# Kernel tuning notes

Measured on AMD Instinct MI355X. Metric: run time of the kernel, lower is better.

## Reference

```python
import jax, jax.numpy as jnp
import numpy as np

INPUT_DIM = 512
N_TREES = 64
TREE_DEPTH = 3
N_LEAVES = 2 ** TREE_DEPTH      # 8
N_INTERNAL = 2 ** TREE_DEPTH - 1  # 7
PPT = N_INTERNAL * (INPUT_DIM + 1) + N_LEAVES * 2  # params per tree = 3607
BATCH = 65536


def setup_inputs() -> dict:
    key = jax.random.key(0)
    k1, k2, k3 = jax.random.split(key, 3)
    x = jax.random.normal(k1, (BATCH, INPUT_DIM), dtype=jnp.float32)
    tree_params = jax.random.normal(k2, (1, N_TREES * PPT), dtype=jnp.float32)
    tree_weights = jax.random.normal(k3, (1, N_TREES), dtype=jnp.float32)
    return {"x": x, "tree_params": tree_params, "tree_weights": tree_weights}


def reference(x, tree_params, tree_weights):
    # Unpack all trees at once: [T, ppt]
    p = tree_params[0].reshape(N_TREES, PPT)
    split_w = p[:, : N_INTERNAL * INPUT_DIM].reshape(N_TREES, N_INTERNAL, INPUT_DIM)
    split_b = p[:, N_INTERNAL * INPUT_DIM : N_INTERNAL * (INPUT_DIM + 1)]  # [T, I]
    leaf_logits = p[:, N_INTERNAL * (INPUT_DIM + 1) :].reshape(N_TREES, N_LEAVES, 2)

    # decisions: [B, T, I]
    decisions = jax.nn.sigmoid(jnp.einsum('bd,tid->bti', x, split_w) + split_b[None])

    # Replicate the original indexing quirk: leaf_probs column j (a tree NODE index)
    # gets factor d_i if j == 2i+1 (and j < n_leaves), (1-d_i) if j == 2i+2.
    # Column 0 remains 1.0; each other column gets exactly one factor.
    cols = []
    for j in range(N_LEAVES):
        if j == 0:
            cols.append(jnp.ones_like(decisions[:, :, 0]))
        elif j % 2 == 1:
            i = (j - 1) // 2
            cols.append(decisions[:, :, i] if i < N_INTERNAL else jnp.ones_like(decisions[:, :, 0]))
        else:
            i = (j - 2) // 2
            cols.append(1.0 - decisions[:, :, i] if i < N_INTERNAL else jnp.ones_like(decisions[:, :, 0]))
    leaf_probs = jnp.stack(cols, axis=-1)  # [B, T, L]
    leaf_probs = leaf_probs / (leaf_probs.sum(axis=-1, keepdims=True) + 1e-8)

    leaf_dist = jax.nn.softmax(leaf_logits, axis=-1)  # [T, L, 2]
    tree_out = jnp.einsum('btl,tlc->btc', leaf_probs, leaf_dist)  # [B, T, 2]
    return jnp.einsum('btc,t->bc', tree_out, tree_weights[0])  # [B, 2]
```

## Files before the change

### kernel.cpp

```cpp
#include <hip/hip_runtime.h>
#include <stdint.h>


#define KDIM 512
#define PPT 3607

typedef _Float16 f16x8 __attribute__((ext_vector_type(8)));
typedef float f32x4 __attribute__((ext_vector_type(4)));


__global__ __launch_bounds__(128) void prep_kernel(const float* __restrict__ p,
                                                   const float* __restrict__ tw,
                                                   _Float16* __restrict__ Wh,
                                                   float* __restrict__ biasN,
                                                   float* __restrict__ AB) {
    const int c = blockIdx.x;
    const int t = c >> 2, i = c & 3;
    const float* wsrc = p + t * PPT + i * KDIM;
    for (int k = threadIdx.x; k < KDIM; k += 128)
        Wh[c * KDIM + k] = (_Float16)wsrc[k];
    if (threadIdx.x == 0)
        biasN[c] = p[t * PPT + 7 * KDIM + i];
    if (threadIdx.x == 64 && c < 64) {
        const int tt = c;
        const float* lg = p + tt * PPT + 7 * 513;
        const float w = tw[tt];
        float ld[8][2];
#pragma unroll
        for (int j = 0; j < 8; ++j) {
            float a = lg[2 * j], b = lg[2 * j + 1];
            float m = fmaxf(a, b);
            float e0 = expf(a - m), e1 = expf(b - m);
            float s = e0 + e1;
            ld[j][0] = e0 / s; ld[j][1] = e1 / s;
        }
        float* o = AB + tt * 10;
#pragma unroll
        for (int cc = 0; cc < 2; ++cc) {
            o[0 + cc] = w * (ld[0][cc] + ld[2][cc] + ld[4][cc] + ld[6][cc]);
            o[2 + cc] = w * (ld[1][cc] - ld[2][cc]);
            o[4 + cc] = w * (ld[3][cc] - ld[4][cc]);
            o[6 + cc] = w * (ld[5][cc] - ld[6][cc]);
            o[8 + cc] = w * (ld[7][cc]);
        }
    }
}

#define BUF_STRIDE 32768
#define W_OFF 16384
#define EPI_STRIDE 260
#define AB_OFF 66560
#define PART_OFF 69120
#define LDS_BYTES 73216

__device__ __forceinline__ void gll16(const void* g, void* l) {
    __builtin_amdgcn_global_load_lds((const __attribute__((address_space(1))) uint32_t*)g,
                                     (__attribute__((address_space(3))) uint32_t*)l, 16, 0, 0);
}

__global__ __launch_bounds__(512, 4) void main_kernel(const float* __restrict__ X,
                                                      const _Float16* __restrict__ Wh,
                                                      const float* __restrict__ biasN,
                                                      const float* __restrict__ ABg,
                                                      float* __restrict__ out) {
    extern __shared__ char smem[];
    const int tid = threadIdx.x;
    const int lane = tid & 63;
    const int w = tid >> 6;
    const int wm = w >> 2;
    const int wn = w & 3;
    const int gr0 = blockIdx.x * 128;

    {
        float* abl = (float*)(smem + AB_OFF);
        for (int i = tid; i < 640; i += 512) abl[i] = ABg[i];
    }
    asm volatile("s_waitcnt vmcnt(0)" ::: "memory");

    const float* srcX[2];
    const _Float16* srcW[2];
    int ldoX[2], ldoW[2];
#pragma unroll
    for (int i = 0; i < 2; ++i) {
        int rowX = i * 64 + w * 8 + (lane >> 3);
        int cX = ((lane & 7) << 2) ^ ((rowX & 7) << 2);
        srcX[i] = X + (size_t)(gr0 + rowX) * KDIM + cX;
        ldoX[i] = (i * 512 + w * 64 + lane) * 16;
        int colW = i * 128 + w * 16 + (lane >> 2);
        int kW = ((lane & 3) << 3) ^ (((colW >> 1) & 3) << 3);
        srcW[i] = Wh + (size_t)colW * KDIM + kW;
        ldoW[i] = W_OFF + (i * 512 + w * 64 + lane) * 16;
    }

#define STAGE(kt, b) do {                                   \
        char* _bb = smem + (b) * BUF_STRIDE;                \
        gll16(srcX[0] + (kt) * 32, _bb + ldoX[0]);          \
        gll16(srcX[1] + (kt) * 32, _bb + ldoX[1]);          \
        gll16(srcW[0] + (kt) * 32, _bb + ldoW[0]);          \
        gll16(srcW[1] + (kt) * 32, _bb + ldoW[1]);          \
    } while (0)

    f32x4 acc[4][4];
#pragma unroll
    for (int rt = 0; rt < 4; ++rt)
#pragma unroll
        for (int nt = 0; nt < 4; ++nt)
            acc[rt][nt] = (f32x4){0.f, 0.f, 0.f, 0.f};

    const int kb = (lane >> 4) << 3;
    const int swA = (lane & 7) << 2;
    const int swB = ((lane >> 1) & 3) << 3;
    const int aRowBase = (wm * 64 + (lane & 15)) * 32;
    const int bColBase = (wn * 64 + (lane & 15)) * 32;

    STAGE(0, 0);

    for (int kt = 0; kt < 16; ++kt) {
        const int b = kt & 1;
        __builtin_amdgcn_s_barrier();
        if (kt < 15) {
            STAGE(kt + 1, b ^ 1);
            asm volatile("s_waitcnt vmcnt(4)" ::: "memory");
        } else {
            asm volatile("s_waitcnt vmcnt(0)" ::: "memory");
        }
        __builtin_amdgcn_s_barrier();
        asm volatile("" ::: "memory");

        const float* Xl = (const float*)(smem + b * BUF_STRIDE);
        const _Float16* Wl = (const _Float16*)(smem + b * BUF_STRIDE + W_OFF);

        f16x8 bfr[4];
#pragma unroll
        for (int nt = 0; nt < 4; ++nt)
            bfr[nt] = *(const f16x8*)&Wl[bColBase + nt * 512 + (kb ^ swB)];
#pragma unroll
        for (int rt = 0; rt < 4; ++rt) {
            float4 a0 = *(const float4*)&Xl[aRowBase + rt * 512 + (kb ^ swA)];
            float4 a1 = *(const float4*)&Xl[aRowBase + rt * 512 + ((kb + 4) ^ swA)];
            f16x8 af;
            af[0] = (_Float16)a0.x; af[1] = (_Float16)a0.y;
            af[2] = (_Float16)a0.z; af[3] = (_Float16)a0.w;
            af[4] = (_Float16)a1.x; af[5] = (_Float16)a1.y;
            af[6] = (_Float16)a1.z; af[7] = (_Float16)a1.w;
#pragma unroll
            for (int nt = 0; nt < 4; ++nt)
                acc[rt][nt] = __builtin_amdgcn_mfma_f32_16x16x32_f16(af, bfr[nt], acc[rt][nt], 0, 0, 0);
        }
    }

    __syncthreads();

    for (int p = 0; p < 2; ++p) {
        if (wm == p) {
            float bl[4];
#pragma unroll
            for (int nt = 0; nt < 4; ++nt) bl[nt] = biasN[wn * 64 + nt * 16 + (lane & 15)];
            float* ep = (float*)smem;
#pragma unroll
            for (int rt = 0; rt < 4; ++rt)
#pragma unroll
                for (int nt = 0; nt < 4; ++nt) {
                    const int col = wn * 64 + nt * 16 + (lane & 15);
#pragma unroll
                    for (int reg = 0; reg < 4; ++reg) {
                        const int rowl = rt * 16 + ((lane >> 4) << 2) + reg;
                        float z = acc[rt][nt][reg] + bl[nt];
                        ep[rowl * EPI_STRIDE + col] = __builtin_amdgcn_rcpf(1.f + __expf(-z));
                    }
                }
        }
        __syncthreads();
        {
            const float* ep = (const float*)smem;
            const float* abl = (const float*)(smem + AB_OFF);
            float* pb = (float*)(smem + PART_OFF);
            const int r = lane;
            float s0 = 0.f, s1 = 0.f;
#pragma unroll
            for (int j = 0; j < 8; ++j) {
                const int t = w * 8 + j;
                float4 dv = *(const float4*)&ep[r * EPI_STRIDE + t * 4];
                const float* abt = &abl[t * 10];
                float inv = __builtin_amdgcn_rcpf(4.f + dv.w + 1e-8f);
                s0 += (abt[0] + dv.x * abt[2] + dv.y * abt[4] + dv.z * abt[6] + dv.w * abt[8]) * inv;
                s1 += (abt[1] + dv.x * abt[3] + dv.y * abt[5] + dv.z * abt[7] + dv.w * abt[9]) * inv;
            }
            pb[(w * 64 + r) * 2 + 0] = s0;
            pb[(w * 64 + r) * 2 + 1] = s1;
        }
        __syncthreads();
        if (tid < 128) {
            const float* pb = (const float*)(smem + PART_OFF);
            const int r = tid >> 1, c = tid & 1;
            float s = 0.f;
#pragma unroll
            for (int g = 0; g < 8; ++g) s += pb[(g * 64 + r) * 2 + c];
            out[(size_t)(gr0 + p * 64 + r) * 2 + c] = s;
        }
        if (p == 0) __syncthreads();
    }
#undef STAGE
}

extern "C" void kernel_launch(void* const* d_in, const int* in_sizes, int n_in,
                              void* d_out, int out_size, void* d_ws, size_t ws_size,
                              hipStream_t stream) {
    const float* x  = (const float*)d_in[0];
    const float* tp = (const float*)d_in[1];
    const float* tw = (const float*)d_in[2];
    float* out = (float*)d_out;

    _Float16* Wh = (_Float16*)d_ws;
    float* biasN = (float*)((char*)d_ws + 262144);
    float* AB    = (float*)((char*)d_ws + 263168);

    (void)hipFuncSetAttribute((const void*)reinterpret_cast<const void*>(&main_kernel),
                              hipFuncAttributeMaxDynamicSharedMemorySize, LDS_BYTES);

    prep_kernel<<<256, 128, 0, stream>>>(tp, tw, Wh, biasN, AB);
    main_kernel<<<512, 512, LDS_BYTES, stream>>>(x, Wh, biasN, AB, out);
}
```

Baseline: 41.93 us.

## Load X through registers, convert to fp16 once, and triple-buffer W

X tiles now go from global memory into registers two stages ahead, are converted to fp16 once per thread, and are written to a smaller double-buffered LDS area. Each wave used to convert the fp32 LDS data itself, so the same values were converted repeatedly. W moves to a three-stage LDS ring loaded two iterations ahead, which allows a single barrier per k-step instead of two. The change trades higher register pressure and more complex vmcnt accounting for fewer barriers, less LDS traffic and fewer conversion instructions.

Result: no change. 42.37 us (+1.0%).

```diff
diff --git a/kernel.cpp b/kernel.cpp
--- a/kernel.cpp
+++ b/kernel.cpp
@@ -46,8 +46,9 @@
     }
 }
 
-#define BUF_STRIDE 32768
-#define W_OFF 16384
+#define XBUF_STRIDE 8192
+#define W_BASE 16384
+#define WBUF_STRIDE 16384
 #define EPI_STRIDE 260
 #define AB_OFF 66560
 #define PART_OFF 69120
@@ -56,6 +57,13 @@
 __device__ __forceinline__ void gll16(const void* g, void* l) {
     __builtin_amdgcn_global_load_lds((const __attribute__((address_space(1))) uint32_t*)g,
                                      (__attribute__((address_space(3))) uint32_t*)l, 16, 0, 0);
+}
+
+__device__ __forceinline__ f16x8 cvt8(float4 a, float4 b) {
+    f16x8 h;
+    h[0] = (_Float16)a.x; h[1] = (_Float16)a.y; h[2] = (_Float16)a.z; h[3] = (_Float16)a.w;
+    h[4] = (_Float16)b.x; h[5] = (_Float16)b.y; h[6] = (_Float16)b.z; h[7] = (_Float16)b.w;
+    return h;
 }
 
 __global__ __launch_bounds__(512, 4) void main_kernel(const float* __restrict__ X,
@@ -77,28 +85,24 @@
     }
     asm volatile("s_waitcnt vmcnt(0)" ::: "memory");
 
-    const float* srcX[2];
+    const float* Xrow = X + (size_t)(gr0 + (tid >> 2)) * KDIM + (tid & 3) * 8;
+    const int wOffX = ((tid >> 2) << 6) + ((((tid & 3) ^ ((tid >> 3) & 3))) << 4);
+
     const _Float16* srcW[2];
-    int ldoX[2], ldoW[2];
+    int dW[2];
 #pragma unroll
     for (int i = 0; i < 2; ++i) {
-        int rowX = i * 64 + w * 8 + (lane >> 3);
-        int cX = ((lane & 7) << 2) ^ ((rowX & 7) << 2);
-        srcX[i] = X + (size_t)(gr0 + rowX) * KDIM + cX;
-        ldoX[i] = (i * 512 + w * 64 + lane) * 16;
         int colW = i * 128 + w * 16 + (lane >> 2);
         int kW = ((lane & 3) << 3) ^ (((colW >> 1) & 3) << 3);
         srcW[i] = Wh + (size_t)colW * KDIM + kW;
-        ldoW[i] = W_OFF + (i * 512 + w * 64 + lane) * 16;
-    }
-
-#define STAGE(kt, b) do {                                   \
-        char* _bb = smem + (b) * BUF_STRIDE;                \
-        gll16(srcX[0] + (kt) * 32, _bb + ldoX[0]);          \
-        gll16(srcX[1] + (kt) * 32, _bb + ldoX[1]);          \
-        gll16(srcW[0] + (kt) * 32, _bb + ldoW[0]);          \
-        gll16(srcW[1] + (kt) * 32, _bb + ldoW[1]);          \
-    } while (0)
+        dW[i] = (i * 512 + w * 64 + lane) * 16;
+    }
+
+    const int kb = (lane >> 4) << 3;
+    const int kws = kb ^ (((lane >> 1) & 3) << 3);
+    const int bColBase = (wn * 64 + (lane & 15)) * 32;
+    const int aOff = ((lane & 15) << 6)
+                   + (((lane >> 4) ^ (((lane & 15) >> 1) & 3)) << 4);
 
     f32x4 acc[4][4];
 #pragma unroll
@@ -107,45 +111,52 @@
         for (int nt = 0; nt < 4; ++nt)
             acc[rt][nt] = (f32x4){0.f, 0.f, 0.f, 0.f};
 
-    const int kb = (lane >> 4) << 3;
-    const int swA = (lane & 7) << 2;
-    const int swB = ((lane >> 1) & 3) << 3;
-    const int aRowBase = (wm * 64 + (lane & 15)) * 32;
-    const int bColBase = (wn * 64 + (lane & 15)) * 32;
-
-    STAGE(0, 0);
-
+    float4 xr[2][2];
+
+    {
+        float4 x0a = *(const float4*)(Xrow + 0);
+        float4 x0b = *(const float4*)(Xrow + 4);
+        gll16(srcW[0] + 0 * 32, smem + W_BASE + 0 * WBUF_STRIDE + dW[0]);
+        gll16(srcW[1] + 0 * 32, smem + W_BASE + 0 * WBUF_STRIDE + dW[1]);
+        xr[1][0] = *(const float4*)(Xrow + 1 * 32);
+        xr[1][1] = *(const float4*)(Xrow + 1 * 32 + 4);
+        gll16(srcW[0] + 1 * 32, smem + W_BASE + 1 * WBUF_STRIDE + dW[0]);
+        gll16(srcW[1] + 1 * 32, smem + W_BASE + 1 * WBUF_STRIDE + dW[1]);
+        *(f16x8*)(smem + 0 * XBUF_STRIDE + wOffX) = cvt8(x0a, x0b);
+    }
+
+#pragma unroll 16
     for (int kt = 0; kt < 16; ++kt) {
-        const int b = kt & 1;
+        if (kt <= 13) {
+            xr[kt & 1][0] = *(const float4*)(Xrow + (kt + 2) * 32);
+            xr[kt & 1][1] = *(const float4*)(Xrow + (kt + 2) * 32 + 4);
+        }
+        if (kt <= 13)      asm volatile("s_waitcnt vmcnt(4)" ::: "memory");
+        else if (kt == 14) asm volatile("s_waitcnt vmcnt(2)" ::: "memory");
+        else               asm volatile("s_waitcnt vmcnt(0)" ::: "memory");
         __builtin_amdgcn_s_barrier();
-        if (kt < 15) {
-            STAGE(kt + 1, b ^ 1);
-            asm volatile("s_waitcnt vmcnt(4)" ::: "memory");
-        } else {
-            asm volatile("s_waitcnt vmcnt(0)" ::: "memory");
-        }
-        __builtin_amdgcn_s_barrier();
-        asm volatile("" ::: "memory");
-
-        const float* Xl = (const float*)(smem + b * BUF_STRIDE);
-        const _Float16* Wl = (const _Float16*)(smem + b * BUF_STRIDE + W_OFF);
-
-        f16x8 bfr[4];
-#pragma unroll
-        for (int nt = 0; nt < 4; ++nt)
-            bfr[nt] = *(const f16x8*)&Wl[bColBase + nt * 512 + (kb ^ swB)];
-#pragma unroll
-        for (int rt = 0; rt < 4; ++rt) {
-            float4 a0 = *(const float4*)&Xl[aRowBase + rt * 512 + (kb ^ swA)];
-            float4 a1 = *(const float4*)&Xl[aRowBase + rt * 512 + ((kb + 4) ^ swA)];
-            f16x8 af;
-            af[0] = (_Float16)a0.x; af[1] = (_Float16)a0.y;
-            af[2] = (_Float16)a0.z; af[3] = (_Float16)a0.w;
-            af[4] = (_Float16)a1.x; af[5] = (_Float16)a1.y;
-            af[6] = (_Float16)a1.z; af[7] = (_Float16)a1.w;
+        if (kt <= 13) {
+            char* wb = smem + W_BASE + ((kt + 2) % 3) * WBUF_STRIDE;
+            gll16(srcW[0] + (kt + 2) * 32, wb + dW[0]);
+            gll16(srcW[1] + (kt + 2) * 32, wb + dW[1]);
+        }
+        if (kt <= 14)
+            *(f16x8*)(smem + ((kt + 1) & 1) * XBUF_STRIDE + wOffX) =
+                cvt8(xr[(kt + 1) & 1][0], xr[(kt + 1) & 1][1]);
+        {
+            const _Float16* Wl = (const _Float16*)(smem + W_BASE + (kt % 3) * WBUF_STRIDE);
+            const char* Xl = smem + (kt & 1) * XBUF_STRIDE + wm * 4096;
+            f16x8 bfr[4];
 #pragma unroll
             for (int nt = 0; nt < 4; ++nt)
-                acc[rt][nt] = __builtin_amdgcn_mfma_f32_16x16x32_f16(af, bfr[nt], acc[rt][nt], 0, 0, 0);
+                bfr[nt] = *(const f16x8*)&Wl[bColBase + nt * 512 + kws];
+#pragma unroll
+            for (int rt = 0; rt < 4; ++rt) {
+                f16x8 af = *(const f16x8*)(Xl + rt * 1024 + aOff);
+#pragma unroll
+                for (int nt = 0; nt < 4; ++nt)
+                    acc[rt][nt] = __builtin_amdgcn_mfma_f32_16x16x32_f16(af, bfr[nt], acc[rt][nt], 0, 0, 0);
+            }
         }
     }
 
@@ -200,7 +211,6 @@
         }
         if (p == 0) __syncthreads();
     }
-#undef STAGE
 }
 
 extern "C" void kernel_launch(void* const* d_in, const int* in_sizes, int n_in,
```

## Keep split weights in registers and stream X through LDS as fp16

Applied to the files above, without the earlier changes.

Each wave now loads its 32 columns of fp16 split weights into registers once, for the whole K dimension. Blocks then stream 256 rows of X in 32-row panels: values are loaded to registers, converted to fp16 and written to a double-buffered swizzled LDS tile, and the MFMA and epilogue run per panel. This drops the per-k-step reload of W from LDS and halves X's LDS footprint. It also gives up the async global_load_lds pipeline, adds a large register cost (Wf is 128 VGPRs, with occupancy lowered to 2 blocks), and adds more barriers per panel.

Result: slower. 47.62 us (+13.6%).

```diff
diff --git a/kernel.cpp b/kernel.cpp
--- a/kernel.cpp
+++ b/kernel.cpp
@@ -4,10 +4,16 @@
 
 #define KDIM 512
 #define PPT 3607
+#define NP 8
+#define EPI_S 260
+#define E_OFF 65536
+#define P_OFF 98816
+#define P_S 34
+#define AB_OFF 103168
+#define LDS_BYTES 105728
 
 typedef _Float16 f16x8 __attribute__((ext_vector_type(8)));
 typedef float f32x4 __attribute__((ext_vector_type(4)));
-
 
 __global__ __launch_bounds__(128) void prep_kernel(const float* __restrict__ p,
                                                    const float* __restrict__ tw,
@@ -46,19 +52,14 @@
     }
 }
 
-#define BUF_STRIDE 32768
-#define W_OFF 16384
-#define EPI_STRIDE 260
-#define AB_OFF 66560
-#define PART_OFF 69120
-#define LDS_BYTES 73216
-
-__device__ __forceinline__ void gll16(const void* g, void* l) {
-    __builtin_amdgcn_global_load_lds((const __attribute__((address_space(1))) uint32_t*)g,
-                                     (__attribute__((address_space(3))) uint32_t*)l, 16, 0, 0);
-}
-
-__global__ __launch_bounds__(512, 4) void main_kernel(const float* __restrict__ X,
+__device__ __forceinline__ f16x8 cvt8(float4 a, float4 b) {
+    f16x8 h;
+    h[0] = (_Float16)a.x; h[1] = (_Float16)a.y; h[2] = (_Float16)a.z; h[3] = (_Float16)a.w;
+    h[4] = (_Float16)b.x; h[5] = (_Float16)b.y; h[6] = (_Float16)b.z; h[7] = (_Float16)b.w;
+    return h;
+}
+
+__global__ __launch_bounds__(512, 2) void main_kernel(const float* __restrict__ X,
                                                       const _Float16* __restrict__ Wh,
                                                       const float* __restrict__ biasN,
                                                       const float* __restrict__ ABg,
@@ -66,141 +67,124 @@
     extern __shared__ char smem[];
     const int tid = threadIdx.x;
     const int lane = tid & 63;
-    const int w = tid >> 6;
-    const int wm = w >> 2;
-    const int wn = w & 3;
-    const int gr0 = blockIdx.x * 128;
+    const int wn = tid >> 6;
+    const int r15 = lane & 15;
+    const int hi = lane >> 4;
+    const int gr0 = blockIdx.x * 256;
 
     {
         float* abl = (float*)(smem + AB_OFF);
         for (int i = tid; i < 640; i += 512) abl[i] = ABg[i];
     }
-    asm volatile("s_waitcnt vmcnt(0)" ::: "memory");
-
-    const float* srcX[2];
-    const _Float16* srcW[2];
-    int ldoX[2], ldoW[2];
-#pragma unroll
-    for (int i = 0; i < 2; ++i) {
-        int rowX = i * 64 + w * 8 + (lane >> 3);
-        int cX = ((lane & 7) << 2) ^ ((rowX & 7) << 2);
-        srcX[i] = X + (size_t)(gr0 + rowX) * KDIM + cX;
-        ldoX[i] = (i * 512 + w * 64 + lane) * 16;
-        int colW = i * 128 + w * 16 + (lane >> 2);
-        int kW = ((lane & 3) << 3) ^ (((colW >> 1) & 3) << 3);
-        srcW[i] = Wh + (size_t)colW * KDIM + kW;
-        ldoW[i] = W_OFF + (i * 512 + w * 64 + lane) * 16;
-    }
-
-#define STAGE(kt, b) do {                                   \
-        char* _bb = smem + (b) * BUF_STRIDE;                \
-        gll16(srcX[0] + (kt) * 32, _bb + ldoX[0]);          \
-        gll16(srcX[1] + (kt) * 32, _bb + ldoX[1]);          \
-        gll16(srcW[0] + (kt) * 32, _bb + ldoW[0]);          \
-        gll16(srcW[1] + (kt) * 32, _bb + ldoW[1]);          \
-    } while (0)
-
-    f32x4 acc[4][4];
-#pragma unroll
-    for (int rt = 0; rt < 4; ++rt)
-#pragma unroll
-        for (int nt = 0; nt < 4; ++nt)
-            acc[rt][nt] = (f32x4){0.f, 0.f, 0.f, 0.f};
-
-    const int kb = (lane >> 4) << 3;
-    const int swA = (lane & 7) << 2;
-    const int swB = ((lane >> 1) & 3) << 3;
-    const int aRowBase = (wm * 64 + (lane & 15)) * 32;
-    const int bColBase = (wn * 64 + (lane & 15)) * 32;
-
-    STAGE(0, 0);
-
-    for (int kt = 0; kt < 16; ++kt) {
-        const int b = kt & 1;
+
+    f16x8 Wf[16][2];
+#pragma unroll
+    for (int s = 0; s < 16; ++s)
+#pragma unroll
+        for (int ct = 0; ct < 2; ++ct)
+            Wf[s][ct] = *(const f16x8*)&Wh[(size_t)(wn * 32 + ct * 16 + r15) * KDIM + s * 32 + hi * 8];
+
+    float bl[2];
+#pragma unroll
+    for (int ct = 0; ct < 2; ++ct) bl[ct] = biasN[wn * 32 + ct * 16 + r15];
+
+    int srow[4], ldw[4];
+#pragma unroll
+    for (int i = 0; i < 4; ++i) {
+        int chunk = i * 512 + tid;
+        int row = chunk >> 6, g = chunk & 63;
+        srow[i] = chunk * 8;
+        ldw[i] = row * 1024 + ((g ^ (row & 15)) << 4);
+    }
+
+    const int aoff0 = r15 * 1024;
+    const int aoff1 = (16 + r15) * 1024;
+
+    const float* Xblk = X + (size_t)gr0 * KDIM;
+    float4 xr[8];
+
+#pragma unroll
+    for (int i = 0; i < 4; ++i) {
+        xr[2 * i]     = *(const float4*)(Xblk + srow[i]);
+        xr[2 * i + 1] = *(const float4*)(Xblk + srow[i] + 4);
+    }
+
+    for (int p = 0; p < NP; ++p) {
+        char* xb = smem + (p & 1) * 32768;
+#pragma unroll
+        for (int i = 0; i < 4; ++i)
+            *(f16x8*)(xb + ldw[i]) = cvt8(xr[2 * i], xr[2 * i + 1]);
+        if (p + 1 < NP) {
+            const float* Xp = Xblk + (size_t)(p + 1) * 32 * KDIM;
+#pragma unroll
+            for (int i = 0; i < 4; ++i) {
+                xr[2 * i]     = *(const float4*)(Xp + srow[i]);
+                xr[2 * i + 1] = *(const float4*)(Xp + srow[i] + 4);
+            }
+        }
+        asm volatile("s_waitcnt lgkmcnt(0)" ::: "memory");
         __builtin_amdgcn_s_barrier();
-        if (kt < 15) {
-            STAGE(kt + 1, b ^ 1);
-            asm volatile("s_waitcnt vmcnt(4)" ::: "memory");
-        } else {
-            asm volatile("s_waitcnt vmcnt(0)" ::: "memory");
-        }
+
+        f32x4 acc[2][2];
+#pragma unroll
+        for (int rt = 0; rt < 2; ++rt)
+#pragma unroll
+            for (int ct = 0; ct < 2; ++ct)
+                acc[rt][ct] = (f32x4){0.f, 0.f, 0.f, 0.f};
+#pragma unroll
+        for (int s = 0; s < 16; ++s) {
+            const int go = ((s * 4 + hi) ^ r15) << 4;
+            f16x8 a0 = *(const f16x8*)(xb + aoff0 + go);
+            f16x8 a1 = *(const f16x8*)(xb + aoff1 + go);
+            acc[0][0] = __builtin_amdgcn_mfma_f32_16x16x32_f16(a0, Wf[s][0], acc[0][0], 0, 0, 0);
+            acc[0][1] = __builtin_amdgcn_mfma_f32_16x16x32_f16(a0, Wf[s][1], acc[0][1], 0, 0, 0);
+            acc[1][0] = __builtin_amdgcn_mfma_f32_16x16x32_f16(a1, Wf[s][0], acc[1][0], 0, 0, 0);
+            acc[1][1] = __builtin_amdgcn_mfma_f32_16x16x32_f16(a1, Wf[s][1], acc[1][1], 0, 0, 0);
+        }
+
+        float* Ef = (float*)(smem + E_OFF);
+#pragma unroll
+        for (int rt = 0; rt < 2; ++rt)
+#pragma unroll
+            for (int ct = 0; ct < 2; ++ct) {
+                const int col = wn * 32 + ct * 16 + r15;
+#pragma unroll
+                for (int reg = 0; reg < 4; ++reg) {
+                    const int row = rt * 16 + hi * 4 + reg;
+                    float z = acc[rt][ct][reg] + bl[ct];
+                    Ef[row * EPI_S + col] = __builtin_amdgcn_rcpf(1.f + __expf(-z));
+                }
+            }
+        asm volatile("s_waitcnt lgkmcnt(0)" ::: "memory");
         __builtin_amdgcn_s_barrier();
-        asm volatile("" ::: "memory");
-
-        const float* Xl = (const float*)(smem + b * BUF_STRIDE);
-        const _Float16* Wl = (const _Float16*)(smem + b * BUF_STRIDE + W_OFF);
-
-        f16x8 bfr[4];
-#pragma unroll
-        for (int nt = 0; nt < 4; ++nt)
-            bfr[nt] = *(const f16x8*)&Wl[bColBase + nt * 512 + (kb ^ swB)];
-#pragma unroll
-        for (int rt = 0; rt < 4; ++rt) {
-            float4 a0 = *(const float4*)&Xl[aRowBase + rt * 512 + (kb ^ swA)];
-            float4 a1 = *(const float4*)&Xl[aRowBase + rt * 512 + ((kb + 4) ^ swA)];
-            f16x8 af;
-            af[0] = (_Float16)a0.x; af[1] = (_Float16)a0.y;
-            af[2] = (_Float16)a0.z; af[3] = (_Float16)a0.w;
-            af[4] = (_Float16)a1.x; af[5] = (_Float16)a1.y;
-            af[6] = (_Float16)a1.z; af[7] = (_Float16)a1.w;
-#pragma unroll
-            for (int nt = 0; nt < 4; ++nt)
-                acc[rt][nt] = __builtin_amdgcn_mfma_f32_16x16x32_f16(af, bfr[nt], acc[rt][nt], 0, 0, 0);
-        }
-    }
-
-    __syncthreads();
-
-    for (int p = 0; p < 2; ++p) {
-        if (wm == p) {
-            float bl[4];
-#pragma unroll
-            for (int nt = 0; nt < 4; ++nt) bl[nt] = biasN[wn * 64 + nt * 16 + (lane & 15)];
-            float* ep = (float*)smem;
-#pragma unroll
-            for (int rt = 0; rt < 4; ++rt)
-#pragma unroll
-                for (int nt = 0; nt < 4; ++nt) {
-                    const int col = wn * 64 + nt * 16 + (lane & 15);
-#pragma unroll
-                    for (int reg = 0; reg < 4; ++reg) {
-                        const int rowl = rt * 16 + ((lane >> 4) << 2) + reg;
-                        float z = acc[rt][nt][reg] + bl[nt];
-                        ep[rowl * EPI_STRIDE + col] = __builtin_amdgcn_rcpf(1.f + __expf(-z));
-                    }
-                }
-        }
-        __syncthreads();
         {
-            const float* ep = (const float*)smem;
             const float* abl = (const float*)(smem + AB_OFF);
-            float* pb = (float*)(smem + PART_OFF);
-            const int r = lane;
+            float* Pf = (float*)(smem + P_OFF);
+            const int row = tid >> 4, tg = tid & 15;
             float s0 = 0.f, s1 = 0.f;
 #pragma unroll
-            for (int j = 0; j < 8; ++j) {
-                const int t = w * 8 + j;
-                float4 dv = *(const float4*)&ep[r * EPI_STRIDE + t * 4];
+            for (int j = 0; j < 4; ++j) {
+                const int t = tg * 4 + j;
+                float4 dv = *(const float4*)&Ef[row * EPI_S + t * 4];
                 const float* abt = &abl[t * 10];
                 float inv = __builtin_amdgcn_rcpf(4.f + dv.w + 1e-8f);
                 s0 += (abt[0] + dv.x * abt[2] + dv.y * abt[4] + dv.z * abt[6] + dv.w * abt[8]) * inv;
                 s1 += (abt[1] + dv.x * abt[3] + dv.y * abt[5] + dv.z * abt[7] + dv.w * abt[9]) * inv;
             }
-            pb[(w * 64 + r) * 2 + 0] = s0;
-            pb[(w * 64 + r) * 2 + 1] = s1;
-        }
-        __syncthreads();
-        if (tid < 128) {
-            const float* pb = (const float*)(smem + PART_OFF);
-            const int r = tid >> 1, c = tid & 1;
+            Pf[row * P_S + tg * 2 + 0] = s0;
+            Pf[row * P_S + tg * 2 + 1] = s1;
+        }
+        asm volatile("s_waitcnt lgkmcnt(0)" ::: "memory");
+        __builtin_amdgcn_s_barrier();
+        if (tid < 64) {
+            const float* Pf = (const float*)(smem + P_OFF);
+            const int row = tid >> 1, c = tid & 1;
             float s = 0.f;
 #pragma unroll
-            for (int g = 0; g < 8; ++g) s += pb[(g * 64 + r) * 2 + c];
-            out[(size_t)(gr0 + p * 64 + r) * 2 + c] = s;
-        }
-        if (p == 0) __syncthreads();
-    }
-#undef STAGE
+            for (int tg = 0; tg < 16; ++tg) s += Pf[row * P_S + tg * 2 + c];
+            out[(size_t)(gr0 + p * 32 + row) * 2 + c] = s;
+        }
+    }
 }
 
 extern "C" void kernel_launch(void* const* d_in, const int* in_sizes, int n_in,
@@ -219,5 +203,5 @@
                               hipFuncAttributeMaxDynamicSharedMemorySize, LDS_BYTES);
 
     prep_kernel<<<256, 128, 0, stream>>>(tp, tw, Wh, biasN, AB);
-    main_kernel<<<512, 512, LDS_BYTES, stream>>>(x, Wh, biasN, AB, out);
-}
+    main_kernel<<<256, 512, LDS_BYTES, stream>>>(x, Wh, biasN, AB, out);
+}
```
